# Performance work log

Hardware: AMD Instinct MI355X
Metric: run time of the kernel (lower is better)

Reference implementation:

```python
import jax, jax.numpy as jnp
import numpy as np

D_MODEL = 1024
H = 16
D_K = D_MODEL // H


def setup_inputs() -> dict:
    key = jax.random.key(0)
    ks = jax.random.split(key, 8)
    B, S = 4, 2048
    q = jax.random.normal(ks[0], (B, S, D_MODEL), dtype=jnp.float32)
    k = jax.random.normal(ks[1], (B, S, D_MODEL), dtype=jnp.float32)
    v = jax.random.normal(ks[2], (B, S, D_MODEL), dtype=jnp.float32)
    scale = 1.0 / np.sqrt(D_MODEL)
    W_q = jax.random.normal(ks[3], (H, D_MODEL, D_K), dtype=jnp.float32) * scale
    W_k = jax.random.normal(ks[4], (H, D_MODEL, D_K), dtype=jnp.float32) * scale
    W_v = jax.random.normal(ks[5], (H, D_MODEL, D_K), dtype=jnp.float32) * scale
    W_o = jax.random.normal(ks[6], (D_MODEL, H * D_K), dtype=jnp.float32) * scale
    b_o = jax.random.normal(ks[7], (D_MODEL,), dtype=jnp.float32) * 0.01
    return {"q": q, "k": k, "v": v, "W_q": W_q, "W_k": W_k, "W_v": W_v, "W_o": W_o, "b_o": b_o}


def reference(q, k, v, W_q, W_k, W_v, W_o, b_o):
    # Per-head projections: [B,S,D] x [H,D,dk] -> [H,B,S,dk]
    qh = jnp.einsum('bsd,hdk->hbsk', q, W_q)
    kh = jnp.einsum('bsd,hdk->hbsk', k, W_k)
    vh = jnp.einsum('bsd,hdk->hbsk', v, W_v)
    # Scaled dot-product attention (full score matrix, as in original)
    scores = jnp.einsum('hbsk,hbtk->hbst', qh, kh) / jnp.sqrt(jnp.asarray(D_K, qh.dtype))
    attn = jax.nn.softmax(scores, axis=-1)
    out = jnp.einsum('hbst,hbtk->hbsk', attn, vh)  # [H,B,S,dk]
    # torch.cat(chunks along head dim, dim=2): head-major feature concat -> [B,S,H*dk]
    out = jnp.transpose(out, (1, 2, 0, 3)).reshape(q.shape[0], q.shape[1], H * D_K)
    return out @ W_o.T + b_o
```

## Files before the change

### kernel.cpp

```cpp
#include <hip/hip_runtime.h>

#define S_LEN 2048

typedef __attribute__((ext_vector_type(8))) short v8s;
typedef __attribute__((ext_vector_type(4))) short v4s;
typedef __attribute__((ext_vector_type(4))) float f32x4;
typedef __attribute__((ext_vector_type(4))) unsigned short v4us;
typedef __attribute__((ext_vector_type(4))) unsigned int v4u;

static __device__ __forceinline__ unsigned short f2bf(float x){
  unsigned u = __builtin_bit_cast(unsigned, x);
  u = (u + 0x7fffu + ((u >> 16) & 1u)) >> 16;
  return (unsigned short)u;
}

static __device__ __forceinline__ unsigned pk2(float a, float b){
  unsigned ua = __builtin_bit_cast(unsigned, a) + 0x8000u;
  unsigned ub = __builtin_bit_cast(unsigned, b) + 0x8000u;
  return __builtin_amdgcn_perm(ub, ua, 0x07060302u);
}

static __device__ __forceinline__ void gload16(const void* g, void* l){
  __builtin_amdgcn_global_load_lds((const __attribute__((address_space(1))) void*)g,
                                   (__attribute__((address_space(3))) void*)l, 16, 0, 0);
}

static __device__ __forceinline__ unsigned lds_off(const void* p){
  return (unsigned)(unsigned long long)(__attribute__((address_space(3))) const void*)p;
}


__global__ void conv_w(const float* __restrict__ Wq, const float* __restrict__ Wk,
                       const float* __restrict__ Wv, const float* __restrict__ Wo,
                       unsigned short* __restrict__ outW){
  int i = blockIdx.x*256 + threadIdx.x;
  const int stride = gridDim.x*256;
  for(; i < 4*1048576; i += stride){
    if (i < 3*1048576){
      int which = i >> 20;
      int rem = i & 1048575;
      const float* W = which==0 ? Wq : (which==1 ? Wk : Wv);
      float v = W[rem];
      if (which == 0) v *= 0.18033688011112042f;
      int h = rem >> 16, d = (rem >> 6) & 1023, kk = rem & 63;
      outW[(which<<20) + (((h<<6)+kk)<<10) + d] = f2bf(v);
    } else {
      outW[i] = f2bf(Wo[i - 3*1048576]);
    }
  }
}

__global__ void conv_x(const float* __restrict__ in, unsigned short* __restrict__ out){
  int i = blockIdx.x*256 + threadIdx.x;
  const int stride = gridDim.x*256;
  const int n4 = 8388608/4;
  for(; i < n4; i += stride){
    float4 v = ((const float4*)in)[i];
    v4us o = { f2bf(v.x), f2bf(v.y), f2bf(v.z), f2bf(v.w) };
    *(v4us*)(out + i*4) = o;
  }
}

template<int EPI>
__global__ __launch_bounds__(256,2) void gemm_bt(const unsigned short* __restrict__ A,
                                                 const unsigned short* __restrict__ Bt,
                                                 void* __restrict__ Cout,
                                                 const float* __restrict__ bias){
  __shared__ unsigned short Als[128*64];
  __shared__ unsigned short Bls[128*64];
  const int tid = threadIdx.x;
  const int l = tid & 63, w = tid >> 6;
  int lid = blockIdx.y*8 + blockIdx.x;
  int nid = (lid & 7)*64 + (lid >> 3);
  const int tx = nid & 7, ty = nid >> 3;
  const int m0 = ty*128, n0 = tx*128;
  const int wr = w >> 1, wc = w & 1;

  f32x4 zero = {0.f,0.f,0.f,0.f};
  f32x4 acc[4][4];
  #pragma unroll
  for(int i=0;i<4;i++){
    #pragma unroll
    for(int j=0;j<4;j++) acc[i][j] = zero;
  }

  const int xorm = (l&7)<<4;
  const int g8 = (l>>4)<<3;
  const int rsub = l>>3, csub = l&7;
  const unsigned short* Abase = A + m0*1024;
  const unsigned short* Bbase = Bt + n0*1024;

  for(int kt=0; kt<16; ++kt){
    const int k0 = kt*64;
    #pragma unroll
    for(int i=0;i<4;i++){
      int c = w*4+i, r = c*8+rsub, col = csub ^ (r&7);
      gload16(Abase + r*1024 + k0 + col*8, (void*)&Als[c*512]);
    }
    #pragma unroll
    for(int i=0;i<4;i++){
      int c = w*4+i, r = c*8+rsub, col = csub ^ (r&7);
      gload16(Bbase + r*1024 + k0 + col*8, (void*)&Bls[c*512]);
    }
    __syncthreads();
    const char* Ab = (const char*)Als;
    const char* Bb = (const char*)Bls;
    #pragma unroll
    for(int kk=0; kk<2; ++kk){
      v8s af[4], bfr[4];
      #pragma unroll
      for(int mf=0; mf<4; ++mf){
        int rb = (wr*64 + mf*16 + (l&15))*128;
        v4s lo = *(const v4s*)(Ab + rb + ((kk*64 + g8) ^ xorm));
        v4s hi = *(const v4s*)(Ab + rb + ((kk*64 + 32 + g8) ^ xorm));
        af[mf] = __builtin_shufflevector(lo, hi, 0,1,2,3,4,5,6,7);
      }
      #pragma unroll
      for(int nf=0; nf<4; ++nf){
        int rb = (wc*64 + nf*16 + (l&15))*128;
        v4s lo = *(const v4s*)(Bb + rb + ((kk*64 + g8) ^ xorm));
        v4s hi = *(const v4s*)(Bb + rb + ((kk*64 + 32 + g8) ^ xorm));
        bfr[nf] = __builtin_shufflevector(lo, hi, 0,1,2,3,4,5,6,7);
      }
      #pragma unroll
      for(int mf=0; mf<4; ++mf){
        #pragma unroll
        for(int nf=0; nf<4; ++nf)
          acc[mf][nf] = __builtin_amdgcn_mfma_f32_16x16x32_bf16(af[mf], bfr[nf], acc[mf][nf], 0,0,0);
      }
    }
    __syncthreads();
  }

  const int g4 = (l>>4)<<2;
  if (EPI == 0){
    unsigned short* C = (unsigned short*)Cout;
    #pragma unroll
    for(int mf=0; mf<4; ++mf){
      int rowb = m0 + wr*64 + mf*16 + g4;
      #pragma unroll
      for(int nf=0; nf<4; ++nf){
        int col = n0 + wc*64 + nf*16 + (l&15);
        #pragma unroll
        for(int r=0;r<4;++r)
          C[(rowb+r)*1024 + col] = f2bf(acc[mf][nf][r]);
      }
    }
  } else {
    float* C = (float*)Cout;
    #pragma unroll
    for(int mf=0; mf<4; ++mf){
      int rowb = m0 + wr*64 + mf*16 + g4;
      #pragma unroll
      for(int nf=0; nf<4; ++nf){
        int col = n0 + wc*64 + nf*16 + (l&15);
        float bv = bias[col];
        #pragma unroll
        for(int r=0;r<4;++r)
          C[(rowb+r)*1024 + col] = acc[mf][nf][r] + bv;
      }
    }
  }
}

__global__ __launch_bounds__(256,2) void attn_fwd(const unsigned short* __restrict__ Q,
                                                  const unsigned short* __restrict__ K,
                                                  const unsigned short* __restrict__ V,
                                                  unsigned short* __restrict__ O){
  __shared__ unsigned short KVls[2][2][64*64];
  const int tid = threadIdx.x;
  const int l = tid & 63, w = tid >> 6;
  int lid = blockIdx.y*16 + blockIdx.x;
  int nid = (lid & 7)*128 + (lid >> 3);
  const int qb = nid & 15, bh = nid >> 4;
  const int b = bh >> 4, h = bh & 15;
  const int base = b*S_LEN*1024 + h*64;
  const int q0 = qb*128;
  const int xorm = (l&7)<<4, g8 = (l>>4)<<3, g4 = (l>>4)<<2;
  const int rsub = l>>3, csub = l&7;

  auto stage_kv = [&](int kt2, int buf){
    const int k0 = kt2*64;
    #pragma unroll
    for(int i=0;i<2;i++){
      int c = w*2+i, r = c*8+rsub, col = csub ^ (r&7);
      gload16(K + base + (k0+r)*1024 + col*8, (void*)&KVls[buf][0][c*512]);
    }
    #pragma unroll
    for(int i=0;i<2;i++){
      int c = w*2+i;
      int e0 = c*512 + l*8;
      int kg = e0>>10, dg = (e0>>8)&3, kin = (e0>>4)&15, din = e0&15;
      gload16(V + base + (k0 + kg*16 + kin)*1024 + dg*16 + din, (void*)&KVls[buf][1][c*512]);
    }
  };

  #pragma unroll
  for(int i=0;i<4;i++){
    int c = w*4+i, r = c*8+rsub, col = csub ^ (r&7);
    gload16(Q + base + (q0+r)*1024 + col*8, (void*)&KVls[1][0][c*512]);
  }
  stage_kv(0, 0);
  __syncthreads();

  v8s qf[2][2];
  {
    const char* Qb = (const char*)&KVls[1][0][0];
    #pragma unroll
    for(int qh=0; qh<2; ++qh){
      int rb = (w*32 + qh*16 + (l&15))*128;
      #pragma unroll
      for(int t=0;t<2;t++){
        v4s lo = *(const v4s*)(Qb + rb + ((t*64 + g8) ^ xorm));
        v4s hi = *(const v4s*)(Qb + rb + ((t*64 + 32 + g8) ^ xorm));
        qf[qh][t] = __builtin_shufflevector(lo, hi, 0,1,2,3,4,5,6,7);
      }
    }
  }
  __builtin_amdgcn_sched_barrier(0);
  __syncthreads();

  f32x4 zero = {0.f,0.f,0.f,0.f};
  f32x4 oacc[2][4];
  #pragma unroll
  for(int qh=0;qh<2;qh++){
    #pragma unroll
    for(int nf=0;nf<4;nf++) oacc[qh][nf] = zero;
  }
  float lsum[2] = {0.f, 0.f};
  const unsigned vbase0 = lds_off(&KVls[0][1][0]) + l*8;
  const unsigned vbase1 = lds_off(&KVls[1][1][0]) + l*8;

  int cur = 0;
  for(int kt=0; kt<32; ++kt){
    if (kt < 31) stage_kv(kt+1, cur^1);

    const char* Kb = (const char*)&KVls[cur][0][0];
    f32x4 sf[2][4];
    #pragma unroll
    for(int mf=0;mf<4;mf++){
      int rb = (mf*16 + (l&15))*128;
      v8s kf[2];
      #pragma unroll
      for(int t=0;t<2;t++){
        v4s lo = *(const v4s*)(Kb + rb + ((t*64 + g8) ^ xorm));
        v4s hi = *(const v4s*)(Kb + rb + ((t*64 + 32 + g8) ^ xorm));
        kf[t] = __builtin_shufflevector(lo, hi, 0,1,2,3,4,5,6,7);
      }
      #pragma unroll
      for(int qh=0;qh<2;qh++){
        sf[qh][mf] = __builtin_amdgcn_mfma_f32_16x16x32_bf16(kf[0], qf[qh][0], zero, 0,0,0);
        sf[qh][mf] = __builtin_amdgcn_mfma_f32_16x16x32_bf16(kf[1], qf[qh][1], sf[qh][mf], 0,0,0);
      }
    }

    const unsigned vb_sel = cur ? vbase1 : vbase0;
    v4s vtr[2][2][4];
    #define TRR(T,H,N,OFF) asm volatile("ds_read_b64_tr_b16 %0, %1 offset:" #OFF \
                     : "=v"(vtr[T][H][N]) : "v"(vb_sel) : "memory")
    TRR(0,0,0,0);    TRR(0,0,1,512);  TRR(0,0,2,1024); TRR(0,0,3,1536);
    TRR(0,1,0,2048); TRR(0,1,1,2560); TRR(0,1,2,3072); TRR(0,1,3,3584);
    TRR(1,0,0,4096); TRR(1,0,1,4608); TRR(1,0,2,5120); TRR(1,0,3,5632);
    TRR(1,1,0,6144); TRR(1,1,1,6656); TRR(1,1,2,7168); TRR(1,1,3,7680);
    #undef TRR

    v8s pa[2][2];
    #pragma unroll
    for(int qh=0;qh<2;qh++){
      unsigned pd[2][4];
      float ls = 0.f;
      #pragma unroll
      for(int mf=0;mf<4;mf++){
        float e0 = __builtin_amdgcn_exp2f(sf[qh][mf][0]);
        float e1 = __builtin_amdgcn_exp2f(sf[qh][mf][1]);
        float e2 = __builtin_amdgcn_exp2f(sf[qh][mf][2]);
        float e3 = __builtin_amdgcn_exp2f(sf[qh][mf][3]);
        ls += (e0+e1)+(e2+e3);
        int t = mf>>1, hf = mf&1;
        pd[t][hf*2+0] = pk2(e0, e1);
        pd[t][hf*2+1] = pk2(e2, e3);
      }
      lsum[qh] += ls;
      #pragma unroll
      for(int t=0;t<2;t++){
        v4u u = { pd[t][0], pd[t][1], pd[t][2], pd[t][3] };
        pa[qh][t] = __builtin_bit_cast(v8s, u);
      }
    }

    asm volatile("s_waitcnt lgkmcnt(0)" ::: "memory");
    __builtin_amdgcn_sched_barrier(0);
    __builtin_amdgcn_s_setprio(1);
    #pragma unroll
    for(int t=0;t<2;t++){
      #pragma unroll
      for(int nf=0;nf<4;nf++){
        v8s vb = __builtin_shufflevector(vtr[t][0][nf], vtr[t][1][nf], 0,1,2,3,4,5,6,7);
        #pragma unroll
        for(int qh=0;qh<2;qh++)
          oacc[qh][nf] = __builtin_amdgcn_mfma_f32_16x16x32_bf16(pa[qh][t], vb, oacc[qh][nf], 0,0,0);
      }
    }
    __builtin_amdgcn_s_setprio(0);
    __syncthreads();
    cur ^= 1;
  }

  #pragma unroll
  for(int qh=0;qh<2;qh++){
    float s = lsum[qh];
    s += __shfl_xor(s, 16, 64);
    s += __shfl_xor(s, 32, 64);
    float i0 = 1.f/__shfl(s, g4+0, 64);
    float i1 = 1.f/__shfl(s, g4+1, 64);
    float i2 = 1.f/__shfl(s, g4+2, 64);
    float i3 = 1.f/__shfl(s, g4+3, 64);
    const int row = q0 + w*32 + qh*16 + g4;
    #pragma unroll
    for(int nf=0;nf<4;nf++){
      int col = nf*16 + (l&15);
      O[base + (row+0)*1024 + col] = f2bf(oacc[qh][nf][0]*i0);
      O[base + (row+1)*1024 + col] = f2bf(oacc[qh][nf][1]*i1);
      O[base + (row+2)*1024 + col] = f2bf(oacc[qh][nf][2]*i2);
      O[base + (row+3)*1024 + col] = f2bf(oacc[qh][nf][3]*i3);
    }
  }
}

extern "C" void kernel_launch(void* const* d_in, const int* in_sizes, int n_in,
                              void* d_out, int out_size, void* d_ws, size_t ws_size,
                              hipStream_t stream) {
  (void)in_sizes; (void)n_in; (void)out_size;
  const float* q  = (const float*)d_in[0];
  const float* k  = (const float*)d_in[1];
  const float* v  = (const float*)d_in[2];
  const float* Wq = (const float*)d_in[3];
  const float* Wk = (const float*)d_in[4];
  const float* Wv = (const float*)d_in[5];
  const float* Wo = (const float*)d_in[6];
  const float* bo = (const float*)d_in[7];

  if (ws_size < (size_t)37748736*2) return;
  unsigned short* ws  = (unsigned short*)d_ws;
  unsigned short* X   = ws;
  unsigned short* Qh  = ws +  8388608;
  unsigned short* Kh  = ws + 16777216;
  unsigned short* Vh  = ws + 25165824;
  unsigned short* Wt  = ws + 33554432;
  unsigned short* Wqt = Wt;
  unsigned short* Wkt = Wt + 1048576;
  unsigned short* Wvt = Wt + 2097152;
  unsigned short* Wob = Wt + 3145728;

  conv_w<<<dim3(2048), dim3(256), 0, stream>>>(Wq, Wk, Wv, Wo, Wt);

  conv_x<<<dim3(2048), dim3(256), 0, stream>>>(q, X);
  gemm_bt<0><<<dim3(8,64), dim3(256), 0, stream>>>(X, Wqt, (void*)Qh, nullptr);
  conv_x<<<dim3(2048), dim3(256), 0, stream>>>(k, X);
  gemm_bt<0><<<dim3(8,64), dim3(256), 0, stream>>>(X, Wkt, (void*)Kh, nullptr);
  conv_x<<<dim3(2048), dim3(256), 0, stream>>>(v, X);
  gemm_bt<0><<<dim3(8,64), dim3(256), 0, stream>>>(X, Wvt, (void*)Vh, nullptr);

  attn_fwd<<<dim3(16,64), dim3(256), 0, stream>>>(Qh, Kh, Vh, X);

  gemm_bt<1><<<dim3(8,64), dim3(256), 0, stream>>>(X, Wob, d_out, bo);
}
```

Baseline: 258.6 us.

## Fuse fp32-to-bf16 input conversion into a single batched QKV projection GEMM

```diff
diff --git a/kernel.cpp b/kernel.cpp
--- a/kernel.cpp
+++ b/kernel.cpp
@@ -28,7 +28,6 @@
 static __device__ __forceinline__ unsigned lds_off(const void* p){
   return (unsigned)(unsigned long long)(__attribute__((address_space(3))) const void*)p;
 }
-
 
 __global__ void conv_w(const float* __restrict__ Wq, const float* __restrict__ Wk,
                        const float* __restrict__ Wv, const float* __restrict__ Wo,
@@ -50,14 +49,93 @@
   }
 }
 
-__global__ void conv_x(const float* __restrict__ in, unsigned short* __restrict__ out){
-  int i = blockIdx.x*256 + threadIdx.x;
-  const int stride = gridDim.x*256;
-  const int n4 = 8388608/4;
-  for(; i < n4; i += stride){
-    float4 v = ((const float4*)in)[i];
-    v4us o = { f2bf(v.x), f2bf(v.y), f2bf(v.z), f2bf(v.w) };
-    *(v4us*)(out + i*4) = o;
+__global__ __launch_bounds__(512,2) void gemm_proj(
+    const float* __restrict__ Aq, const float* __restrict__ Ak, const float* __restrict__ Avv,
+    const unsigned short* __restrict__ Wtb,
+    unsigned short* __restrict__ C0, unsigned short* __restrict__ C1, unsigned short* __restrict__ C2){
+  __shared__ unsigned short Als[128*64];
+  __shared__ unsigned short Bls[256*64];
+  const int tid = threadIdx.x;
+  const int l = tid & 63, w = tid >> 6;
+  const int z = blockIdx.z;
+  const float* Af = (z==0) ? Aq : ((z==1) ? Ak : Avv);
+  unsigned short* Cb = (z==0) ? C0 : ((z==1) ? C1 : C2);
+  int lid = blockIdx.y*4 + blockIdx.x;
+  int nid = (lid & 7)*32 + (lid >> 3);
+  const int tx = nid & 3, ty = nid >> 2;
+  const int m0 = ty*128, n0 = tx*256;
+  const int wr = w >> 2, wc = w & 3;
+
+  f32x4 zero = {0.f,0.f,0.f,0.f};
+  f32x4 acc[4][4];
+  #pragma unroll
+  for(int i=0;i<4;i++){
+    #pragma unroll
+    for(int j=0;j<4;j++) acc[i][j] = zero;
+  }
+
+  const int xorm = (l&7)<<4;
+  const int g8 = (l>>4)<<3;
+  const int rsub = l>>3, csub = l&7;
+  const float* Abase = Af + m0*1024;
+  const unsigned short* Bbase = Wtb + z*1048576 + n0*1024;
+
+  for(int kt=0; kt<16; ++kt){
+    const int k0 = kt*64;
+    #pragma unroll
+    for(int i=0;i<2;i++){
+      int c = w*2+i, r = c*8+rsub;
+      const float4* src = (const float4*)(Abase + r*1024 + k0 + csub*8);
+      float4 x0 = src[0], x1 = src[1];
+      v4u o = { pk2(x0.x,x0.y), pk2(x0.z,x0.w), pk2(x1.x,x1.y), pk2(x1.z,x1.w) };
+      *(v4u*)&Als[c*512 + rsub*64 + ((csub ^ (r&7))<<3)] = o;
+    }
+    #pragma unroll
+    for(int i=0;i<4;i++){
+      int c = w*4+i, r = c*8+rsub, col = csub ^ (r&7);
+      gload16(Bbase + r*1024 + k0 + col*8, (void*)&Bls[c*512]);
+    }
+    __syncthreads();
+    const char* Ab = (const char*)Als;
+    const char* Bb = (const char*)Bls;
+    #pragma unroll
+    for(int kk=0; kk<2; ++kk){
+      v8s af[4], bfr[4];
+      #pragma unroll
+      for(int mf=0; mf<4; ++mf){
+        int rb = (wr*64 + mf*16 + (l&15))*128;
+        v4s lo = *(const v4s*)(Ab + rb + ((kk*64 + g8) ^ xorm));
+        v4s hi = *(const v4s*)(Ab + rb + ((kk*64 + 32 + g8) ^ xorm));
+        af[mf] = __builtin_shufflevector(lo, hi, 0,1,2,3,4,5,6,7);
+      }
+      #pragma unroll
+      for(int nf=0; nf<4; ++nf){
+        int rb = (wc*64 + nf*16 + (l&15))*128;
+        v4s lo = *(const v4s*)(Bb + rb + ((kk*64 + g8) ^ xorm));
+        v4s hi = *(const v4s*)(Bb + rb + ((kk*64 + 32 + g8) ^ xorm));
+        bfr[nf] = __builtin_shufflevector(lo, hi, 0,1,2,3,4,5,6,7);
+      }
+      #pragma unroll
+      for(int mf=0; mf<4; ++mf){
+        #pragma unroll
+        for(int nf=0; nf<4; ++nf)
+          acc[mf][nf] = __builtin_amdgcn_mfma_f32_16x16x32_bf16(af[mf], bfr[nf], acc[mf][nf], 0,0,0);
+      }
+    }
+    __syncthreads();
+  }
+
+  const int g4 = (l>>4)<<2;
+  #pragma unroll
+  for(int mf=0; mf<4; ++mf){
+    int rowb = m0 + wr*64 + mf*16 + g4;
+    #pragma unroll
+    for(int nf=0; nf<4; ++nf){
+      int col = n0 + wc*64 + nf*16 + (l&15);
+      #pragma unroll
+      for(int r=0;r<4;++r)
+        Cb[(rowb+r)*1024 + col] = f2bf(acc[mf][nf][r]);
+    }
   }
 }
 
@@ -342,26 +420,18 @@
 
   if (ws_size < (size_t)37748736*2) return;
   unsigned short* ws  = (unsigned short*)d_ws;
-  unsigned short* X   = ws;
-  unsigned short* Qh  = ws +  8388608;
-  unsigned short* Kh  = ws + 16777216;
-  unsigned short* Vh  = ws + 25165824;
+  unsigned short* Qh  = ws;
+  unsigned short* Kh  = ws +  8388608;
+  unsigned short* Vh  = ws + 16777216;
+  unsigned short* AO  = ws + 25165824;
   unsigned short* Wt  = ws + 33554432;
-  unsigned short* Wqt = Wt;
-  unsigned short* Wkt = Wt + 1048576;
-  unsigned short* Wvt = Wt + 2097152;
   unsigned short* Wob = Wt + 3145728;
 
   conv_w<<<dim3(2048), dim3(256), 0, stream>>>(Wq, Wk, Wv, Wo, Wt);
 
-  conv_x<<<dim3(2048), dim3(256), 0, stream>>>(q, X);
-  gemm_bt<0><<<dim3(8,64), dim3(256), 0, stream>>>(X, Wqt, (void*)Qh, nullptr);
-  conv_x<<<dim3(2048), dim3(256), 0, stream>>>(k, X);
-  gemm_bt<0><<<dim3(8,64), dim3(256), 0, stream>>>(X, Wkt, (void*)Kh, nullptr);
-  conv_x<<<dim3(2048), dim3(256), 0, stream>>>(v, X);
-  gemm_bt<0><<<dim3(8,64), dim3(256), 0, stream>>>(X, Wvt, (void*)Vh, nullptr);
-
-  attn_fwd<<<dim3(16,64), dim3(256), 0, stream>>>(Qh, Kh, Vh, X);
-
-  gemm_bt<1><<<dim3(8,64), dim3(256), 0, stream>>>(X, Wob, d_out, bo);
-}
+  gemm_proj<<<dim3(4,64,3), dim3(512), 0, stream>>>(q, k, v, Wt, Qh, Kh, Vh);
+
+  attn_fwd<<<dim3(16,64), dim3(256), 0, stream>>>(Qh, Kh, Vh, AO);
+
+  gemm_bt<1><<<dim3(8,64), dim3(256), 0, stream>>>(AO, Wob, d_out, bo);
+}
```

Result: faster. 235.8 us (-8.8%).
